# Kernel tuning notes

Measured on AMD Instinct MI355X. Metric: run time of the kernel, lower is better.

Reference implementation:

```python
import jax, jax.numpy as jnp
import numpy as np

WS = 7          # window size
NH = 12         # num heads
EPS = 1e-5      # LayerNorm eps
LS_INIT = 1e-5  # layer-scale init value


def _rel_index(ws):
    # Swin relative-position index, computed with numpy (static constant).
    coords = np.stack(np.meshgrid(np.arange(ws), np.arange(ws), indexing='ij'))  # (2, ws, ws)
    flat = coords.reshape(2, -1)                                                 # (2, ws*ws)
    rel = flat[:, :, None] - flat[:, None, :]                                    # (2, N, N)
    rel = rel.transpose(1, 2, 0).copy()                                          # (N, N, 2)
    rel[..., 0] += ws - 1
    rel[..., 1] += ws - 1
    rel[..., 0] *= 2 * ws - 1
    return jnp.asarray(rel.sum(-1))                                              # (N, N) int


def _ln(x, g, b):
    m = jnp.mean(x, axis=-1, keepdims=True)
    v = jnp.mean((x - m) ** 2, axis=-1, keepdims=True)
    return (x - m) * jax.lax.rsqrt(v + EPS) * g + b


def setup_inputs() -> dict:
    key = jax.random.key(0)
    ks = jax.random.split(key, 8)
    B, H, W, C = 8, 56, 56, 384
    L = H * W
    s = 0.05  # weight scale to keep softmax logits in a sane range
    inp = {
        'x': jax.random.normal(ks[0], (B, L, C), jnp.float32),
        'q_w': jax.random.normal(ks[1], (C, C), jnp.float32) * s,
        'kv_w': jax.random.normal(ks[2], (2 * C, C), jnp.float32) * s,
        'proj_w': jax.random.normal(ks[3], (C, C), jnp.float32) * s,
        'proj_b': jnp.zeros((C,), jnp.float32),
        'fc1_w': jax.random.normal(ks[4], (4 * C, C), jnp.float32) * s,
        'fc1_b': jnp.zeros((4 * C,), jnp.float32),
        'fc2_w': jax.random.normal(ks[5], (C, 4 * C), jnp.float32) * s,
        'fc2_b': jnp.zeros((C,), jnp.float32),
        'norm1_g': jnp.ones((C,), jnp.float32),
        'norm1_b': jnp.zeros((C,), jnp.float32),
        'norm2_g': jnp.ones((C,), jnp.float32),
        'norm2_b': jnp.zeros((C,), jnp.float32),
        'ls1': jnp.full((C,), LS_INIT, jnp.float32),
        'ls2': jnp.full((C,), LS_INIT, jnp.float32),
        'rel_bias_table': jax.random.normal(ks[6], ((2 * WS - 1) ** 2, NH), jnp.float32) * 0.02,
        'H': H,
        'W': W,
    }
    return inp


def reference(x, q_w, kv_w, proj_w, proj_b, fc1_w, fc1_b, fc2_w, fc2_b,
              norm1_g, norm1_b, norm2_g, norm2_b, ls1, ls2, rel_bias_table, H, W):
    B, L, C = x.shape
    ws, nh = WS, NH
    hd = C // nh
    N = ws * ws
    nHw, nWw = H // ws, W // ws

    shortcut = x
    xn = _ln(x, norm1_g, norm1_b)

    # window partition -> (B*nHw*nWw, ws*ws, C)
    xw = xn.reshape(B, nHw, ws, nWw, ws, C).transpose(0, 1, 3, 2, 4, 5).reshape(-1, N, C)
    Bw = xw.shape[0]

    # q / kv projections (torch Linear: y = x @ W.T)
    q = jnp.einsum('bnc,dc->bnd', xw, q_w).reshape(Bw, N, nh, hd).transpose(0, 2, 1, 3)
    kv = jnp.einsum('bnc,dc->bnd', xw, kv_w).reshape(Bw, N, 2, nh, hd).transpose(2, 0, 3, 1, 4)
    k, v = kv[0], kv[1]                         # (Bw, nh, N, hd)

    attn = jnp.einsum('bhnd,bhmd->bhnm', q, k) * (hd ** -0.5)

    idx = _rel_index(ws)                        # (N, N)
    bias = rel_bias_table[idx.reshape(-1)].reshape(N, N, nh).transpose(2, 0, 1)  # (nh, N, N)
    attn = jax.nn.softmax(attn + bias[None], axis=-1)

    o = jnp.einsum('bhnm,bhmd->bhnd', attn, v).transpose(0, 2, 1, 3).reshape(Bw, N, C)
    o = o @ proj_w.T + proj_b

    # window reverse -> (B, L, C)
    o = o.reshape(B, nHw, nWw, ws, ws, C).transpose(0, 1, 3, 2, 4, 5).reshape(B, L, C)

    x = shortcut + ls1 * o
    h = _ln(x, norm2_g, norm2_b)
    h = jax.nn.gelu(h @ fc1_w.T + fc1_b, approximate=False)
    h = h @ fc2_w.T + fc2_b
    return x + ls2 * h
```

## Files before the change

kernel.cpp:

```cpp
#include <hip/hip_runtime.h>
#include <hip/hip_bf16.h>
#include <math.h>

#define T_TOK 25088
#define L_DIM 3136
#define C_DIM 384
#define NHEADS 12
#define HDIM 32
#define NWIN 512
#define NTOK 49

typedef __attribute__((ext_vector_type(8))) short bf16x8_t;
typedef __attribute__((ext_vector_type(4))) float f32x4;

__device__ __forceinline__ float bf2f(unsigned short u) {
    return __uint_as_float(((unsigned)u) << 16);
}
__device__ __forceinline__ unsigned short f2bf(float f) {
    __hip_bfloat16 h = __float2bfloat16(f);
    return *(unsigned short*)&h;
}
__device__ __forceinline__ float gelu_fast(float x) {
    return x / (1.0f + __expf(-1.702f * x));
}

__device__ __forceinline__ void gload_lds16(const unsigned short* g, unsigned short* l) {
    __builtin_amdgcn_global_load_lds(
        (const __attribute__((address_space(1))) unsigned int*)(const void*)g,
        (__attribute__((address_space(3))) unsigned int*)(void*)l,
        16, 0, 0);
}

__global__ __launch_bounds__(256) void convert_weights_kernel(
    const float* __restrict__ qw, const float* __restrict__ kvw,
    const float* __restrict__ pw, const float* __restrict__ f1,
    const float* __restrict__ f2, unsigned short* __restrict__ dst)
{
    int i = blockIdx.x * 256 + threadIdx.x;
    if (i >= 442368) return;
    const float* src; int off;
    if      (i < 36864)  { src = qw;  off = i;          }
    else if (i < 110592) { src = kvw; off = i - 36864;  }
    else if (i < 147456) { src = pw;  off = i - 110592; }
    else if (i < 294912) { src = f1;  off = i - 147456; }
    else                 { src = f2;  off = i - 294912; }
    float4 v = ((const float4*)src)[off];
    unsigned short* d = dst + (size_t)i * 4;
    d[0] = f2bf(v.x); d[1] = f2bf(v.y); d[2] = f2bf(v.z); d[3] = f2bf(v.w);
}

__global__ __launch_bounds__(256) void bias_precompute_kernel(
    const float* __restrict__ table, float* __restrict__ biasmat)
{
    int e = blockIdx.x * 256 + threadIdx.x;
    if (e >= 28812) return;
    int h = e / 2401, r = e % 2401;
    int n = r / 49, m = r % 49;
    int i1 = n / 7, j1 = n % 7, i2 = m / 7, j2 = m % 7;
    int idx = (i1 - i2 + 6) * 13 + (j1 - j2 + 6);
    biasmat[e] = table[idx * NHEADS + h];
}

template<bool WINDOWED, bool OUTB>
__global__ __launch_bounds__(256) void ln_kernel(
    const float* __restrict__ x, const float* __restrict__ g,
    const float* __restrict__ b, void* __restrict__ yv)
{
    int gid  = blockIdx.x * 256 + threadIdx.x;
    int t    = gid >> 6;
    int lane = threadIdx.x & 63;
    if (t >= T_TOK) return;

    const float* row = x + (size_t)t * C_DIM;
    float vals[6];
    float s = 0.f, s2 = 0.f;
#pragma unroll
    for (int i = 0; i < 6; ++i) {
        float v = row[lane + i * 64];
        vals[i] = v; s += v; s2 += v * v;
    }
#pragma unroll
    for (int off = 32; off; off >>= 1) {
        s  += __shfl_down(s, off);
        s2 += __shfl_down(s2, off);
    }
    s  = __shfl(s, 0);
    s2 = __shfl(s2, 0);
    float mean = s * (1.0f / C_DIM);
    float var  = s2 * (1.0f / C_DIM) - mean * mean;
    float rstd = rsqrtf(var + 1e-5f);

    size_t orow;
    if (WINDOWED) {
        int bb = t / L_DIM, l = t % L_DIM;
        int hr = l / 56, wc = l % 56;
        int w  = (bb * 8 + hr / 7) * 8 + wc / 7;
        int n  = (hr % 7) * 7 + (wc % 7);
        orow = ((size_t)w * NTOK + n) * C_DIM;
    } else {
        orow = (size_t)t * C_DIM;
    }
#pragma unroll
    for (int i = 0; i < 6; ++i) {
        int c = lane + i * 64;
        float o = (vals[i] - mean) * rstd * g[c] + b[c];
        if (OUTB) ((unsigned short*)yv)[orow + c] = f2bf(o);
        else      ((float*)yv)[orow + c] = o;
    }
}

template<int EPI, bool OUTB, bool WINREV>
__global__ __launch_bounds__(256) void gemm_bf16_kernel(
    const unsigned short* __restrict__ X, const unsigned short* __restrict__ W,
    const float* __restrict__ bias, const float* __restrict__ res,
    const float* __restrict__ ls, void* __restrict__ Yv,
    int M, int Nn, int K)
{
    __shared__ __align__(16) char smem[32768];
    unsigned short* As0 = (unsigned short*)smem;
    unsigned short* Bs0 = (unsigned short*)(smem + 8192);
    unsigned short* As1 = (unsigned short*)(smem + 16384);
    unsigned short* Bs1 = (unsigned short*)(smem + 24576);
    float* cs = (float*)smem;

    int Nt  = gridDim.y;
    int nwg = gridDim.x * Nt;
    int id  = blockIdx.y * gridDim.x + blockIdx.x;
    int qq  = nwg >> 3, rr = nwg & 7;
    int xcd = id & 7, pos = id >> 3;
    int swz = (xcd < rr) ? (xcd * (qq + 1) + pos)
                         : (rr * (qq + 1) + (xcd - rr) * qq + pos);
    int m0 = (swz / Nt) * 128, n0 = (swz % Nt) * 128;

    int tid  = threadIdx.x;
    int wave = tid >> 6, lane = tid & 63;
    int wr   = wave >> 1, wc = wave & 1;
    int lrow = lane & 15;
    int lk   = (lane >> 4) << 3;

    int srow = tid >> 2;
    int scol = (tid & 3) << 3;

    const unsigned short* Xa = X + (size_t)(m0 + srow) * K + scol;
    const unsigned short* Xb = X + (size_t)(m0 + 64 + srow) * K + scol;
    const unsigned short* Wa = W + (size_t)(n0 + srow) * K + scol;
    const unsigned short* Wb = W + (size_t)(n0 + 64 + srow) * K + scol;

    f32x4 acc[4][4] = {};
    int nt = K >> 5;

    gload_lds16(Xa, As0 + tid * 8);
    gload_lds16(Xb, As0 + 2048 + tid * 8);
    gload_lds16(Wa, Bs0 + tid * 8);
    gload_lds16(Wb, Bs0 + 2048 + tid * 8);
    __syncthreads();

    for (int t = 0; t < nt; ++t) {
        unsigned short* A  = (t & 1) ? As1 : As0;
        unsigned short* B  = (t & 1) ? Bs1 : Bs0;
        if (t + 1 < nt) {
            unsigned short* An = (t & 1) ? As0 : As1;
            unsigned short* Bn = (t & 1) ? Bs0 : Bs1;
            int k0 = (t + 1) << 5;
            gload_lds16(Xa + k0, An + tid * 8);
            gload_lds16(Xb + k0, An + 2048 + tid * 8);
            gload_lds16(Wa + k0, Bn + tid * 8);
            gload_lds16(Wb + k0, Bn + 2048 + tid * 8);
        }

        bf16x8_t av[4], bv[4];
#pragma unroll
        for (int i = 0; i < 4; ++i)
            av[i] = *(const bf16x8_t*)&A[(wr * 64 + i * 16 + lrow) * 32 + lk];
#pragma unroll
        for (int j = 0; j < 4; ++j)
            bv[j] = *(const bf16x8_t*)&B[(wc * 64 + j * 16 + lrow) * 32 + lk];
#pragma unroll
        for (int i = 0; i < 4; ++i)
#pragma unroll
            for (int j = 0; j < 4; ++j)
                acc[i][j] = __builtin_amdgcn_mfma_f32_16x16x32_bf16(
                    av[i], bv[j], acc[i][j], 0, 0, 0);
        __syncthreads();
    }

#pragma unroll
    for (int i = 0; i < 4; ++i) {
#pragma unroll
        for (int j = 0; j < 4; ++j)
#pragma unroll
            for (int q = 0; q < 4; ++q)
                cs[(wr * 16 + ((lane >> 4) << 2) + q) * 132 + wc * 64 + j * 16 + lrow]
                    = acc[i][j][q];
        __syncthreads();
#pragma unroll
        for (int p = 0; p < 2; ++p) {
            int eidx = p * 256 + tid;
            int row  = eidx >> 4;
            int cg   = (eidx & 15) << 3;
            int s    = row >> 4, r = row & 15;
            float v[8];
#pragma unroll
            for (int u = 0; u < 8; ++u) v[u] = cs[(s * 16 + r) * 132 + cg + u];
            int col0 = n0 + cg;
            if (EPI >= 1) {
#pragma unroll
                for (int u = 0; u < 8; ++u) v[u] += bias[col0 + u];
            }
            if (EPI == 2) {
#pragma unroll
                for (int u = 0; u < 8; ++u) v[u] = gelu_fast(v[u]);
            }
            int grow = m0 + s * 64 + i * 16 + r;
            size_t orow;
            if (WINREV) {
                int w = grow / 49, n = grow % 49;
                int bb = w >> 6, rem = w & 63;
                int t = bb * L_DIM + ((rem >> 3) * 7 + n / 7) * 56 + (rem & 7) * 7 + n % 7;
                orow = (size_t)t * Nn;
            } else {
                orow = (size_t)grow * Nn;
            }
            if (EPI == 3) {
#pragma unroll
                for (int u = 0; u < 8; ++u)
                    v[u] = res[orow + col0 + u] + ls[col0 + u] * v[u];
            }
            if (OUTB) {
                bf16x8_t pk;
#pragma unroll
                for (int u = 0; u < 8; ++u) pk[u] = (short)f2bf(v[u]);
                *(bf16x8_t*)((unsigned short*)Yv + orow + col0) = pk;
            } else {
                float4 a = make_float4(v[0], v[1], v[2], v[3]);
                float4 b = make_float4(v[4], v[5], v[6], v[7]);
                *(float4*)((float*)Yv + orow + col0)     = a;
                *(float4*)((float*)Yv + orow + col0 + 4) = b;
            }
        }
        __syncthreads();
    }
}

__global__ __launch_bounds__(64) void attn_mfma_kernel(
    const unsigned short* __restrict__ qkv,
    const float* __restrict__ biasmat,
    unsigned short* __restrict__ o)
{
    __shared__ unsigned short vs[64 * 40];
    __shared__ unsigned short ps[64 * 64];

    int w    = blockIdx.x / NHEADS;
    int h    = blockIdx.x % NHEADS;
    int lane = threadIdx.x;
    int g    = lane >> 4;
    int lr   = lane & 15;

    for (int t = lane; t < 196; t += 64) {
        int row = t >> 2, c = t & 3;
        bf16x8_t v = *(const bf16x8_t*)(qkv + ((size_t)w * NTOK + row) * 1152 + 768 + h * HDIM + c * 8);
        *(bf16x8_t*)(vs + row * 40 + c * 8) = v;
    }
    if (lane < 60) {
        int row = 49 + (lane >> 2), c = lane & 3;
        bf16x8_t z = {};
        *(bf16x8_t*)(vs + row * 40 + c * 8) = z;
    }

    bf16x8_t qf[4], kf[4];
#pragma unroll
    for (int i = 0; i < 4; ++i) {
        int qrow = i * 16 + lr; if (qrow > 48) qrow = 0;
        qf[i] = *(const bf16x8_t*)(qkv + ((size_t)w * NTOK + qrow) * 1152 + h * HDIM + g * 8);
        kf[i] = *(const bf16x8_t*)(qkv + ((size_t)w * NTOK + qrow) * 1152 + 384 + h * HDIM + g * 8);
    }

    f32x4 sacc[4][4];
    const f32x4 zf = {0.f, 0.f, 0.f, 0.f};
#pragma unroll
    for (int i = 0; i < 4; ++i)
#pragma unroll
        for (int j = 0; j < 4; ++j)
            sacc[i][j] = __builtin_amdgcn_mfma_f32_16x16x32_bf16(qf[i], kf[j], zf, 0, 0, 0);

    const float scale = 0.17677669529663687f;
    const float* bh = biasmat + h * 2401;
#pragma unroll
    for (int ni = 0; ni < 4; ++ni) {
#pragma unroll
        for (int q = 0; q < 4; ++q) {
            int row = ni * 16 + g * 4 + q;
            float sv[4];
#pragma unroll
            for (int mj = 0; mj < 4; ++mj) {
                int col = lr + mj * 16;
                float bias = (col < NTOK)
                    ? ((row < NTOK) ? bh[row * NTOK + col] : 0.f)
                    : -INFINITY;
                sv[mj] = sacc[ni][mj][q] * scale + bias;
            }
            float mx = fmaxf(fmaxf(sv[0], sv[1]), fmaxf(sv[2], sv[3]));
#pragma unroll
            for (int d = 1; d < 16; d <<= 1) mx = fmaxf(mx, __shfl_xor(mx, d));
            float e[4], sum = 0.f;
#pragma unroll
            for (int mj = 0; mj < 4; ++mj) {
                int col = lr + mj * 16;
                e[mj] = (col < NTOK) ? expf(sv[mj] - mx) : 0.f;
                sum += e[mj];
            }
#pragma unroll
            for (int d = 1; d < 16; d <<= 1) sum += __shfl_xor(sum, d);
            float rinv = 1.f / sum;
#pragma unroll
            for (int mj = 0; mj < 4; ++mj) {
                int col = lr + mj * 16;
                int byteoff = (row * 128 + col * 2) ^ ((row & 7) << 4);
                *(unsigned short*)((char*)ps + byteoff) = f2bf(e[mj] * rinv);
            }
        }
    }
    __syncthreads();

    f32x4 oacc[4][2] = {};
#pragma unroll
    for (int ks = 0; ks < 2; ++ks) {
        bf16x8_t pf[4];
#pragma unroll
        for (int ni = 0; ni < 4; ++ni) {
            int row = ni * 16 + lr;
            int byteoff = (row * 128 + (ks * 32 + g * 8) * 2) ^ ((row & 7) << 4);
            pf[ni] = *(const bf16x8_t*)((char*)ps + byteoff);
        }
        bf16x8_t vf[2];
#pragma unroll
        for (int dj = 0; dj < 2; ++dj) {
#pragma unroll
            for (int j = 0; j < 8; ++j)
                vf[dj][j] = (short)vs[(ks * 32 + g * 8 + j) * 40 + lr + dj * 16];
        }
#pragma unroll
        for (int ni = 0; ni < 4; ++ni)
#pragma unroll
            for (int dj = 0; dj < 2; ++dj)
                oacc[ni][dj] = __builtin_amdgcn_mfma_f32_16x16x32_bf16(
                    pf[ni], vf[dj], oacc[ni][dj], 0, 0, 0);
    }

#pragma unroll
    for (int ni = 0; ni < 4; ++ni) {
#pragma unroll
        for (int q = 0; q < 4; ++q) {
            int row = ni * 16 + g * 4 + q;
            if (row < NTOK) {
#pragma unroll
                for (int dj = 0; dj < 2; ++dj)
                    o[((size_t)w * NTOK + row) * C_DIM + h * HDIM + lr + dj * 16] =
                        f2bf(oacc[ni][dj][q]);
            }
        }
    }
}

extern "C" void kernel_launch(void* const* d_in, const int* in_sizes, int n_in,
                              void* d_out, int out_size, void* d_ws, size_t ws_size,
                              hipStream_t stream)
{
    const float* x       = (const float*)d_in[0];
    const float* q_w     = (const float*)d_in[1];
    const float* kv_w    = (const float*)d_in[2];
    const float* proj_w  = (const float*)d_in[3];
    const float* proj_b  = (const float*)d_in[4];
    const float* fc1_w   = (const float*)d_in[5];
    const float* fc1_b   = (const float*)d_in[6];
    const float* fc2_w   = (const float*)d_in[7];
    const float* fc2_b   = (const float*)d_in[8];
    const float* n1g     = (const float*)d_in[9];
    const float* n1b     = (const float*)d_in[10];
    const float* n2g     = (const float*)d_in[11];
    const float* n2b     = (const float*)d_in[12];
    const float* ls1     = (const float*)d_in[13];
    const float* ls2     = (const float*)d_in[14];
    const float* btable  = (const float*)d_in[15];

    float* out = (float*)d_out;
    char*  ws  = (char*)d_ws;

    unsigned short* qkvbuf = (unsigned short*)(ws);
    unsigned short* hidden = (unsigned short*)(ws);
    unsigned short* xw     = (unsigned short*)(ws + 115605504);
    unsigned short* obuf   = xw;
    unsigned short* hbuf   = (unsigned short*)(ws + 134873088);
    unsigned short* wqkv   = (unsigned short*)(ws + 154140672);
    unsigned short* wproj  = wqkv + 442368;
    unsigned short* wfc1   = wproj + 147456;
    unsigned short* wfc2   = wfc1 + 589824;
    float*          biasmat= (float*)(ws + 161218560);

    convert_weights_kernel<<<1728, 256, 0, stream>>>(q_w, kv_w, proj_w, fc1_w, fc2_w, wqkv);
    bias_precompute_kernel<<<113, 256, 0, stream>>>(btable, biasmat);

    ln_kernel<true, true><<<(T_TOK * 64 + 255) / 256, 256, 0, stream>>>(x, n1g, n1b, xw);

    gemm_bf16_kernel<0, true, false><<<dim3(T_TOK / 128, 1152 / 128), 256, 0, stream>>>(
        xw, wqkv, nullptr, nullptr, nullptr, qkvbuf, T_TOK, 1152, C_DIM);

    attn_mfma_kernel<<<NWIN * NHEADS, 64, 0, stream>>>(qkvbuf, biasmat, obuf);

    gemm_bf16_kernel<3, false, true><<<dim3(T_TOK / 128, C_DIM / 128), 256, 0, stream>>>(
        obuf, wproj, proj_b, x, ls1, out, T_TOK, C_DIM, C_DIM);

    ln_kernel<false, true><<<(T_TOK * 64 + 255) / 256, 256, 0, stream>>>(out, n2g, n2b, hbuf);

    gemm_bf16_kernel<2, true, false><<<dim3(T_TOK / 128, 1536 / 128), 256, 0, stream>>>(
        hbuf, wfc1, fc1_b, nullptr, nullptr, hidden, T_TOK, 1536, C_DIM);

    gemm_bf16_kernel<3, false, false><<<dim3(T_TOK / 128, C_DIM / 128), 256, 0, stream>>>(
        hidden, wfc2, fc2_b, out, ls2, out, T_TOK, C_DIM, 1536);
}
```

Before: 349.5 us.

## Stage bf16 bias table in LDS and process two windows per attention block

The relative-position bias is now precomputed as bf16 in a padded 52-wide layout and copied into shared memory with direct global-to-LDS loads, instead of each lane reading fp32 bias from global memory. Each attention block now runs two waves that handle two windows of the same head and share that bias tile. V loads are issued into registers before the Q/K loads and written to LDS afterwards, which hides some load latency. Storing the bias in bf16 loses precision in the logits, and the extra block-wide barrier couples the two waves.

After: 340.4 us. -2.6%, faster.

```diff
diff --git a/kernel.cpp b/kernel.cpp
--- a/kernel.cpp
+++ b/kernel.cpp
@@ -50,7 +50,7 @@
 }
 
 __global__ __launch_bounds__(256) void bias_precompute_kernel(
-    const float* __restrict__ table, float* __restrict__ biasmat)
+    const float* __restrict__ table, unsigned short* __restrict__ biasmat16)
 {
     int e = blockIdx.x * 256 + threadIdx.x;
     if (e >= 28812) return;
@@ -58,7 +58,7 @@
     int n = r / 49, m = r % 49;
     int i1 = n / 7, j1 = n % 7, i2 = m / 7, j2 = m % 7;
     int idx = (i1 - i2 + 6) * 13 + (j1 - j2 + 6);
-    biasmat[e] = table[idx * NHEADS + h];
+    biasmat16[h * 2560 + n * 52 + m] = f2bf(table[idx * NHEADS + h]);
 }
 
 template<bool WINDOWED, bool OUTB>
@@ -242,29 +242,40 @@
     }
 }
 
-__global__ __launch_bounds__(64) void attn_mfma_kernel(
+__global__ __launch_bounds__(128) void attn_mfma_kernel(
     const unsigned short* __restrict__ qkv,
-    const float* __restrict__ biasmat,
+    const unsigned short* __restrict__ biasmat16,
     unsigned short* __restrict__ o)
 {
-    __shared__ unsigned short vs[64 * 40];
-    __shared__ unsigned short ps[64 * 64];
-
-    int w    = blockIdx.x / NHEADS;
+    __shared__ unsigned short bias_s[2560];
+    __shared__ unsigned short vs[2][64 * 40];
+    __shared__ unsigned short ps[2][64 * 64];
+
     int h    = blockIdx.x % NHEADS;
-    int lane = threadIdx.x;
+    int w    = (blockIdx.x / NHEADS) * 2 + (threadIdx.x >> 6);
+    int lane = threadIdx.x & 63;
+    int wave = threadIdx.x >> 6;
     int g    = lane >> 4;
     int lr   = lane & 15;
 
-    for (int t = lane; t < 196; t += 64) {
-        int row = t >> 2, c = t & 3;
-        bf16x8_t v = *(const bf16x8_t*)(qkv + ((size_t)w * NTOK + row) * 1152 + 768 + h * HDIM + c * 8);
-        *(bf16x8_t*)(vs + row * 40 + c * 8) = v;
-    }
-    if (lane < 60) {
-        int row = 49 + (lane >> 2), c = lane & 3;
-        bf16x8_t z = {};
-        *(bf16x8_t*)(vs + row * 40 + c * 8) = z;
+    const unsigned short* bsrc = biasmat16 + h * 2560;
+    {
+        int c0 = wave * 64 + lane;
+        gload_lds16(bsrc + c0 * 8, bias_s + c0 * 8);
+        int c1 = 128 + wave * 64 + lane;
+        gload_lds16(bsrc + c1 * 8, bias_s + c1 * 8);
+        int c2 = 256 + wave * 64 + lane;
+        if (c2 < 320)
+            gload_lds16(bsrc + c2 * 8, bias_s + c2 * 8);
+    }
+
+    const unsigned short* vbase = qkv + (size_t)w * NTOK * 1152 + 768 + h * HDIM;
+    bf16x8_t vreg[4];
+#pragma unroll
+    for (int k = 0; k < 4; ++k) {
+        int t = lane + k * 64;
+        if (t < 196)
+            vreg[k] = *(const bf16x8_t*)(vbase + (size_t)(t >> 2) * 1152 + (t & 3) * 8);
     }
 
     bf16x8_t qf[4], kf[4];
@@ -275,6 +286,18 @@
         kf[i] = *(const bf16x8_t*)(qkv + ((size_t)w * NTOK + qrow) * 1152 + 384 + h * HDIM + g * 8);
     }
 
+#pragma unroll
+    for (int k = 0; k < 4; ++k) {
+        int t = lane + k * 64;
+        if (t < 196)
+            *(bf16x8_t*)(vs[wave] + (t >> 2) * 40 + (t & 3) * 8) = vreg[k];
+    }
+    if (lane < 60) {
+        int row = 49 + (lane >> 2), c = lane & 3;
+        bf16x8_t z = {};
+        *(bf16x8_t*)(vs[wave] + row * 40 + c * 8) = z;
+    }
+
     f32x4 sacc[4][4];
     const f32x4 zf = {0.f, 0.f, 0.f, 0.f};
 #pragma unroll
@@ -283,8 +306,9 @@
         for (int j = 0; j < 4; ++j)
             sacc[i][j] = __builtin_amdgcn_mfma_f32_16x16x32_bf16(qf[i], kf[j], zf, 0, 0, 0);
 
+    __syncthreads();
+
     const float scale = 0.17677669529663687f;
-    const float* bh = biasmat + h * 2401;
 #pragma unroll
     for (int ni = 0; ni < 4; ++ni) {
 #pragma unroll
@@ -295,7 +319,7 @@
             for (int mj = 0; mj < 4; ++mj) {
                 int col = lr + mj * 16;
                 float bias = (col < NTOK)
-                    ? ((row < NTOK) ? bh[row * NTOK + col] : 0.f)
+                    ? ((row < NTOK) ? bf2f(bias_s[row * 52 + col]) : 0.f)
                     : -INFINITY;
                 sv[mj] = sacc[ni][mj][q] * scale + bias;
             }
@@ -316,11 +340,10 @@
             for (int mj = 0; mj < 4; ++mj) {
                 int col = lr + mj * 16;
                 int byteoff = (row * 128 + col * 2) ^ ((row & 7) << 4);
-                *(unsigned short*)((char*)ps + byteoff) = f2bf(e[mj] * rinv);
-            }
-        }
-    }
-    __syncthreads();
+                *(unsigned short*)((char*)ps[wave] + byteoff) = f2bf(e[mj] * rinv);
+            }
+        }
+    }
 
     f32x4 oacc[4][2] = {};
 #pragma unroll
@@ -330,14 +353,14 @@
         for (int ni = 0; ni < 4; ++ni) {
             int row = ni * 16 + lr;
             int byteoff = (row * 128 + (ks * 32 + g * 8) * 2) ^ ((row & 7) << 4);
-            pf[ni] = *(const bf16x8_t*)((char*)ps + byteoff);
+            pf[ni] = *(const bf16x8_t*)((char*)ps[wave] + byteoff);
         }
         bf16x8_t vf[2];
 #pragma unroll
         for (int dj = 0; dj < 2; ++dj) {
 #pragma unroll
             for (int j = 0; j < 8; ++j)
-                vf[dj][j] = (short)vs[(ks * 32 + g * 8 + j) * 40 + lr + dj * 16];
+                vf[dj][j] = (short)vs[wave][(ks * 32 + g * 8 + j) * 40 + lr + dj * 16];
         }
 #pragma unroll
         for (int ni = 0; ni < 4; ++ni)
@@ -395,17 +418,17 @@
     unsigned short* wproj  = wqkv + 442368;
     unsigned short* wfc1   = wproj + 147456;
     unsigned short* wfc2   = wfc1 + 589824;
-    float*          biasmat= (float*)(ws + 161218560);
+    unsigned short* biasmat16 = (unsigned short*)(ws + 161218560);
 
     convert_weights_kernel<<<1728, 256, 0, stream>>>(q_w, kv_w, proj_w, fc1_w, fc2_w, wqkv);
-    bias_precompute_kernel<<<113, 256, 0, stream>>>(btable, biasmat);
+    bias_precompute_kernel<<<113, 256, 0, stream>>>(btable, biasmat16);
 
     ln_kernel<true, true><<<(T_TOK * 64 + 255) / 256, 256, 0, stream>>>(x, n1g, n1b, xw);
 
     gemm_bf16_kernel<0, true, false><<<dim3(T_TOK / 128, 1152 / 128), 256, 0, stream>>>(
         xw, wqkv, nullptr, nullptr, nullptr, qkvbuf, T_TOK, 1152, C_DIM);
 
-    attn_mfma_kernel<<<NWIN * NHEADS, 64, 0, stream>>>(qkvbuf, biasmat, obuf);
+    attn_mfma_kernel<<<(NWIN / 2) * NHEADS, 128, 0, stream>>>(qkvbuf, biasmat16, obuf);
 
     gemm_bf16_kernel<3, false, true><<<dim3(T_TOK / 128, C_DIM / 128), 256, 0, stream>>>(
         obuf, wproj, proj_b, x, ls1, out, T_TOK, C_DIM, C_DIM);
```
